# Kernel tuning notes

Measured on AMD Instinct MI355X. Metric: run time of the kernel, lower is better.

## Reference

```python
import jax, jax.numpy as jnp
import numpy as np


def setup_inputs() -> dict:
    key = jax.random.key(0)
    k1, k2 = jax.random.split(key)
    tensor_1 = jax.random.normal(k1, (8192, 256), dtype=jnp.float32)
    tensor_2 = jax.random.normal(k2, (16384, 256), dtype=jnp.float32)
    return {"tensor_1": tensor_1, "tensor_2": tensor_2}


def reference(tensor_1, tensor_2):
    # L2-normalize along the feature dim (matches torch .norm(dim=-1), no eps)
    n1 = tensor_1 / jnp.linalg.norm(tensor_1, axis=-1, keepdims=True)  # [N, d]
    n2 = tensor_2 / jnp.linalg.norm(tensor_2, axis=-1, keepdims=True)  # [M, d]
    cos_sim = jnp.einsum("nd,md->nm", n1, n2)  # [N, M] cosine similarity
    top3, _ = jax.lax.top_k(cos_sim, 3)        # [N, 3]
    return top3.mean(axis=-1)                  # [N]
```

## Files before the change

### kernel.cpp

```cpp
#include <hip/hip_runtime.h>
#include <hip/hip_bf16.h>
#include <stdint.h>

#define N1 8192
#define N2 16384
#define DIM 256
#define NSPLIT 16
#define BM 128
#define BN 128
#define BK 128
#define COLS_PER_SPLIT (N2 / NSPLIT)
#define NT_PER_SPLIT (COLS_PER_SPLIT / BN)
#define NPART (NSPLIT * 2)

typedef short v8s  __attribute__((ext_vector_type(8)));
typedef float f32x4 __attribute__((ext_vector_type(4)));

#define GLD16(g, l)                                                                         \
  __builtin_amdgcn_global_load_lds((const __attribute__((address_space(1))) uint32_t*)(g),  \
                                   (__attribute__((address_space(3))) uint32_t*)(l), 16, 0, 0)

__device__ __forceinline__ void top3_insert(float v, float& t0, float& t1, float& t2) {
    float nt1 = __builtin_amdgcn_fmed3f(v, t0, t1);
    float nt2 = __builtin_amdgcn_fmed3f(v, t1, t2);
    t0 = fmaxf(t0, v);
    t1 = nt1;
    t2 = nt2;
}

__global__ __launch_bounds__(256) void normalize_kernel(
        const float* __restrict__ inA, const float* __restrict__ inB,
        __hip_bfloat16* __restrict__ outA, __hip_bfloat16* __restrict__ outB) {
    const int gw   = blockIdx.x * 4 + (threadIdx.x >> 6);
    const int lane = threadIdx.x & 63;
    const float* in;
    __hip_bfloat16* out;
    int row;
    if (gw < N1) { in = inA; out = outA; row = gw; }
    else         { in = inB; out = outB; row = gw - N1; }
    const float4 v = *(const float4*)(in + (size_t)row * DIM + lane * 4);
    float s = v.x * v.x + v.y * v.y + v.z * v.z + v.w * v.w;
    #pragma unroll
    for (int off = 32; off; off >>= 1) s += __shfl_xor(s, off, 64);
    const float inv = 1.0f / sqrtf(s);
    __hip_bfloat16 o[4];
    o[0] = __float2bfloat16(v.x * inv);
    o[1] = __float2bfloat16(v.y * inv);
    o[2] = __float2bfloat16(v.z * inv);
    o[3] = __float2bfloat16(v.w * inv);
    *(uint2*)(out + (size_t)row * DIM + lane * 4) = *(uint2*)o;
}

__global__ __launch_bounds__(256, 2) void gemm_top3_kernel(
        const __hip_bfloat16* __restrict__ A, const __hip_bfloat16* __restrict__ B,
        float* __restrict__ partial) {
    __shared__ char smem[32768 + 32768];
    char* tileA = smem;
    char* tileB = smem + 32768;

    const int tid  = threadIdx.x;
    const int wave = tid >> 6;
    const int lane = tid & 63;
    const int lo   = lane & 15;
    const int quad = lane >> 4;
    const int rb    = blockIdx.x >> 4;
    const int split = blockIdx.x & 15;
    const int row0 = rb * BM;
    const int C0   = split * COLS_PER_SPLIT;
    const int wr = (wave >> 1) * 64;
    const int wc = (wave & 1) * 64;

    const int lr  = lane >> 4;
    const int s16 = lane & 15;

    const char* Agbase = (const char*)A + ((size_t)(row0 + wave * 32 + lr)) * 512;
    const char* Bgbase = (const char*)B + ((size_t)(C0   + wave * 32 + lr)) * 512;
    char* AldsBase = tileA + wave * 32 * 256;
    char* BldsBase = tileB + wave * 32 * 256;

    int aoff[4], boff[4];
    #pragma unroll
    for (int ks = 0; ks < 4; ks++) {
        const int swz = ((ks * 4 + quad) ^ lo) * 16;
        aoff[ks] = (wr + lo) * 256 + swz;
        boff[ks] = (wc + lo) * 256 + swz;
    }

    float t0[16], t1[16], t2[16];
    #pragma unroll
    for (int i = 0; i < 16; i++) { t0[i] = -1e30f; t1[i] = -1e30f; t2[i] = -1e30f; }

    for (int nt = 0; nt < NT_PER_SPLIT; ++nt) {
        f32x4 acc[4][4];
        #pragma unroll
        for (int kk = 0; kk < 2; kk++) {
            __syncthreads();
            #pragma unroll
            for (int j = 0; j < 8; j++) {
                const int sxj = (s16 ^ ((j * 4 + lr) & 15)) * 16;
                GLD16(Agbase + (size_t)j * 2048 + kk * 256 + sxj, AldsBase + j * 1024);
                GLD16(Bgbase + (size_t)nt * 65536 + (size_t)j * 2048 + kk * 256 + sxj,
                      BldsBase + j * 1024);
            }
            __syncthreads();
            #pragma unroll
            for (int ks = 0; ks < 4; ks++) {
                v8s af[4];
                #pragma unroll
                for (int rt = 0; rt < 4; rt++)
                    af[rt] = *(const v8s*)(tileA + aoff[ks] + rt * 4096);
                #pragma unroll
                for (int ct = 0; ct < 4; ct++) {
                    v8s bf = *(const v8s*)(tileB + boff[ks] + ct * 4096);
                    #pragma unroll
                    for (int rt = 0; rt < 4; rt++) {
                        if (kk == 0 && ks == 0)
                            acc[rt][ct] = __builtin_amdgcn_mfma_f32_16x16x32_bf16(
                                af[rt], bf, (f32x4){0.f, 0.f, 0.f, 0.f}, 0, 0, 0);
                        else
                            acc[rt][ct] = __builtin_amdgcn_mfma_f32_16x16x32_bf16(
                                af[rt], bf, acc[rt][ct], 0, 0, 0);
                    }
                }
            }
        }
        #pragma unroll
        for (int rt = 0; rt < 4; rt++)
            #pragma unroll
            for (int r = 0; r < 4; r++) {
                const int i = rt * 4 + r;
                #pragma unroll
                for (int ct = 0; ct < 4; ct++)
                    top3_insert(acc[rt][ct][r], t0[i], t1[i], t2[i]);
            }
    }

    #pragma unroll
    for (int step = 1; step < 16; step <<= 1) {
        #pragma unroll
        for (int i = 0; i < 16; i++) {
            float b0 = __shfl_xor(t0[i], step, 64);
            float b1 = __shfl_xor(t1[i], step, 64);
            float b2 = __shfl_xor(t2[i], step, 64);
            top3_insert(b0, t0[i], t1[i], t2[i]);
            top3_insert(b1, t0[i], t1[i], t2[i]);
            top3_insert(b2, t0[i], t1[i], t2[i]);
        }
    }

    if (lo == 0) {
        #pragma unroll
        for (int rt = 0; rt < 4; rt++)
            #pragma unroll
            for (int r = 0; r < 4; r++) {
                const int i = rt * 4 + r;
                const int row = row0 + wr + rt * 16 + quad * 4 + r;
                float* p = partial + ((size_t)row * NPART + (split * 2 + (wave & 1))) * 3;
                p[0] = t0[i]; p[1] = t1[i]; p[2] = t2[i];
            }
    }
}

__global__ __launch_bounds__(256) void merge_kernel(
        const float* __restrict__ partial, float* __restrict__ out) {
    const int row = blockIdx.x * 256 + threadIdx.x;
    if (row >= N1) return;
    const float* p = partial + (size_t)row * NPART * 3;
    float t0 = -1e30f, t1 = -1e30f, t2 = -1e30f;
    #pragma unroll
    for (int i = 0; i < NPART * 3; i++) top3_insert(p[i], t0, t1, t2);
    out[row] = (t0 + t1 + t2) * (1.0f / 3.0f);
}

extern "C" void kernel_launch(void* const* d_in, const int* in_sizes, int n_in,
                              void* d_out, int out_size, void* d_ws, size_t ws_size,
                              hipStream_t stream) {
    const float* tA = (const float*)d_in[0];
    const float* tB = (const float*)d_in[1];
    float* out = (float*)d_out;

    __hip_bfloat16* An = (__hip_bfloat16*)d_ws;
    __hip_bfloat16* Bn = An + (size_t)N1 * DIM;
    float* partial = (float*)(Bn + (size_t)N2 * DIM);

    normalize_kernel<<<(N1 + N2) / 4, 256, 0, stream>>>(tA, tB, An, Bn);
    gemm_top3_kernel<<<(N1 / BM) * NSPLIT, 256, 0, stream>>>(An, Bn, partial);
    merge_kernel<<<N1 / 256, 256, 0, stream>>>(partial, out);
}
```

Baseline: 152.5 us.

## Repack normalized operands into MFMA fragment layout and stream B directly from global

The normalize kernel now writes bf16 rows in an MFMA-fragment-ordered layout, so each lane's 16-byte fragment is contiguous. The GEMM keeps half of the A tile in registers and the other half in LDS, loaded once per block. B fragments are read straight from global memory each tile, which removes the per-tile LDS staging and the two barriers per k-chunk. In exchange, B reads depend on global/L2 latency with no software pipelining, and register pressure rises from holding the A fragments.

```diff
diff --git a/kernel.cpp b/kernel.cpp
--- a/kernel.cpp
+++ b/kernel.cpp
@@ -8,9 +8,7 @@
 #define NSPLIT 16
 #define BM 128
 #define BN 128
-#define BK 128
-#define COLS_PER_SPLIT (N2 / NSPLIT)
-#define NT_PER_SPLIT (COLS_PER_SPLIT / BN)
+#define NT_PER_SPLIT 8
 #define NPART (NSPLIT * 2)
 
 typedef short v8s  __attribute__((ext_vector_type(8)));
@@ -28,16 +26,16 @@
     t2 = nt2;
 }
 
-__global__ __launch_bounds__(256) void normalize_kernel(
+__global__ __launch_bounds__(256) void normalize_repack_kernel(
         const float* __restrict__ inA, const float* __restrict__ inB,
-        __hip_bfloat16* __restrict__ outA, __hip_bfloat16* __restrict__ outB) {
+        char* __restrict__ Af, char* __restrict__ Bf) {
     const int gw   = blockIdx.x * 4 + (threadIdx.x >> 6);
     const int lane = threadIdx.x & 63;
     const float* in;
-    __hip_bfloat16* out;
+    char* dst;
     int row;
-    if (gw < N1) { in = inA; out = outA; row = gw; }
-    else         { in = inB; out = outB; row = gw - N1; }
+    if (gw < N1) { in = inA; dst = Af; row = gw; }
+    else         { in = inB; dst = Bf; row = gw - N1; }
     const float4 v = *(const float4*)(in + (size_t)row * DIM + lane * 4);
     float s = v.x * v.x + v.y * v.y + v.z * v.z + v.w * v.w;
     #pragma unroll
@@ -48,15 +46,19 @@
     o[1] = __float2bfloat16(v.y * inv);
     o[2] = __float2bfloat16(v.z * inv);
     o[3] = __float2bfloat16(v.w * inv);
-    *(uint2*)(out + (size_t)row * DIM + lane * 4) = *(uint2*)o;
+    const int t    = row >> 4;
+    const int lo   = row & 15;
+    const int ks   = lane >> 3;
+    const int quad = (lane >> 1) & 3;
+    const int half = lane & 1;
+    const size_t off = ((size_t)(t * 8 + ks) * 64 + quad * 16 + lo) * 16 + half * 8;
+    *(uint2*)(dst + off) = *(uint2*)o;
 }
 
 __global__ __launch_bounds__(256, 2) void gemm_top3_kernel(
-        const __hip_bfloat16* __restrict__ A, const __hip_bfloat16* __restrict__ B,
+        const char* __restrict__ Af, const char* __restrict__ Bf,
         float* __restrict__ partial) {
-    __shared__ char smem[32768 + 32768];
-    char* tileA = smem;
-    char* tileB = smem + 32768;
+    __shared__ char smem[32768];
 
     const int tid  = threadIdx.x;
     const int wave = tid >> 6;
@@ -66,61 +68,49 @@
     const int rb    = blockIdx.x >> 4;
     const int split = blockIdx.x & 15;
     const int row0 = rb * BM;
-    const int C0   = split * COLS_PER_SPLIT;
+    const int C0   = split * (N2 / NSPLIT);
     const int wr = (wave >> 1) * 64;
     const int wc = (wave & 1) * 64;
+    const int wt = wr >> 4;
 
-    const int lr  = lane >> 4;
-    const int s16 = lane & 15;
-
-    const char* Agbase = (const char*)A + ((size_t)(row0 + wave * 32 + lr)) * 512;
-    const char* Bgbase = (const char*)B + ((size_t)(C0   + wave * 32 + lr)) * 512;
-    char* AldsBase = tileA + wave * 32 * 256;
-    char* BldsBase = tileB + wave * 32 * 256;
-
-    int aoff[4], boff[4];
+    const char* Ablk = Af + (size_t)(row0 >> 4) * 8192;
     #pragma unroll
-    for (int ks = 0; ks < 4; ks++) {
-        const int swz = ((ks * 4 + quad) ^ lo) * 16;
-        aoff[ks] = (wr + lo) * 256 + swz;
-        boff[ks] = (wc + lo) * 256 + swz;
-    }
+    for (int j = 0; j < 8; j++)
+        GLD16(Ablk + (size_t)j * 8192 + 4096 + tid * 16, smem + j * 4096 + tid * 16);
+    v8s areg[4][4];
+    #pragma unroll
+    for (int rt = 0; rt < 4; rt++)
+        #pragma unroll
+        for (int ks = 0; ks < 4; ks++)
+            areg[rt][ks] = *(const v8s*)(Ablk + (size_t)((wt + rt) * 8 + ks) * 1024 + lane * 16);
+    __syncthreads();
 
     float t0[16], t1[16], t2[16];
     #pragma unroll
     for (int i = 0; i < 16; i++) { t0[i] = -1e30f; t1[i] = -1e30f; t2[i] = -1e30f; }
 
     for (int nt = 0; nt < NT_PER_SPLIT; ++nt) {
+        const char* Bb = Bf + ((size_t)((C0 >> 4) + nt * 8 + (wc >> 4))) * 8192 + lane * 16;
         f32x4 acc[4][4];
         #pragma unroll
-        for (int kk = 0; kk < 2; kk++) {
-            __syncthreads();
+        for (int ks = 0; ks < 8; ks++) {
+            v8s af[4];
             #pragma unroll
-            for (int j = 0; j < 8; j++) {
-                const int sxj = (s16 ^ ((j * 4 + lr) & 15)) * 16;
-                GLD16(Agbase + (size_t)j * 2048 + kk * 256 + sxj, AldsBase + j * 1024);
-                GLD16(Bgbase + (size_t)nt * 65536 + (size_t)j * 2048 + kk * 256 + sxj,
-                      BldsBase + j * 1024);
-            }
-            __syncthreads();
+            for (int rt = 0; rt < 4; rt++)
+                af[rt] = (ks < 4)
+                    ? areg[rt][ks]
+                    : *(const v8s*)(smem + (size_t)((wt + rt) * 4 + (ks - 4)) * 1024 + lane * 16);
             #pragma unroll
-            for (int ks = 0; ks < 4; ks++) {
-                v8s af[4];
+            for (int ct = 0; ct < 4; ct++) {
+                v8s bf = *(const v8s*)(Bb + (size_t)ct * 8192 + ks * 1024);
                 #pragma unroll
-                for (int rt = 0; rt < 4; rt++)
-                    af[rt] = *(const v8s*)(tileA + aoff[ks] + rt * 4096);
-                #pragma unroll
-                for (int ct = 0; ct < 4; ct++) {
-                    v8s bf = *(const v8s*)(tileB + boff[ks] + ct * 4096);
-                    #pragma unroll
-                    for (int rt = 0; rt < 4; rt++) {
-                        if (kk == 0 && ks == 0)
-                            acc[rt][ct] = __builtin_amdgcn_mfma_f32_16x16x32_bf16(
-                                af[rt], bf, (f32x4){0.f, 0.f, 0.f, 0.f}, 0, 0, 0);
-                        else
-                            acc[rt][ct] = __builtin_amdgcn_mfma_f32_16x16x32_bf16(
-                                af[rt], bf, acc[rt][ct], 0, 0, 0);
-                    }
+                for (int rt = 0; rt < 4; rt++) {
+                    if (ks == 0)
+                        acc[rt][ct] = __builtin_amdgcn_mfma_f32_16x16x32_bf16(
+                            af[rt], bf, (f32x4){0.f, 0.f, 0.f, 0.f}, 0, 0, 0);
+                    else
+                        acc[rt][ct] = __builtin_amdgcn_mfma_f32_16x16x32_bf16(
+                            af[rt], bf, acc[rt][ct], 0, 0, 0);
                 }
             }
         }
@@ -179,11 +169,11 @@
     const float* tB = (const float*)d_in[1];
     float* out = (float*)d_out;
 
-    __hip_bfloat16* An = (__hip_bfloat16*)d_ws;
-    __hip_bfloat16* Bn = An + (size_t)N1 * DIM;
-    float* partial = (float*)(Bn + (size_t)N2 * DIM);
+    char* Af = (char*)d_ws;
+    char* Bf = Af + (size_t)N1 * DIM * 2;
+    float* partial = (float*)(Bf + (size_t)N2 * DIM * 2);
 
-    normalize_kernel<<<(N1 + N2) / 4, 256, 0, stream>>>(tA, tB, An, Bn);
-    gemm_top3_kernel<<<(N1 / BM) * NSPLIT, 256, 0, stream>>>(An, Bn, partial);
+    normalize_repack_kernel<<<(N1 + N2) / 4, 256, 0, stream>>>(tA, tB, Af, Bf);
+    gemm_top3_kernel<<<(N1 / BM) * NSPLIT, 256, 0, stream>>>(Af, Bf, partial);
     merge_kernel<<<N1 / 256, 256, 0, stream>>>(partial, out);
 }
```

New measurement: 242.4 us. 58.9% more time.
